# Performance work log

Measured on AMD Instinct MI355X. Metric: run time of the kernel, lower is better.

Reference implementation:

```python
import jax, jax.numpy as jnp
import numpy as np

EPS_FEAT = 1.0 + 1e-4   # feature_map offset: elu(x) + 1.0 + 0.0001
EPS_DEN = 1e-6


def setup_inputs() -> dict:
    key = jax.random.key(0)
    k1, k2, k3 = jax.random.split(key, 3)
    B, L, D = 4, 4096, 1024
    x = jax.random.normal(k1, (B, L, D), dtype=jnp.float32)
    # torch Linear-style init scale ~ 1/sqrt(fan_in)
    W_qkv = jax.random.normal(k2, (D, 3 * D), dtype=jnp.float32) / np.sqrt(D)
    b_qkv = jnp.zeros((3 * D,), dtype=jnp.float32)
    W_out = jax.random.normal(k3, (D, D), dtype=jnp.float32) / np.sqrt(D)
    b_out = jnp.zeros((D,), dtype=jnp.float32)
    return {"x": x, "W_qkv": W_qkv, "b_qkv": b_qkv, "W_out": W_out, "b_out": b_out}


def _linear_attention(x, W_qkv, b_qkv, W_out, b_out, num_heads=16):
    B, L, D = x.shape
    H = num_heads
    E = D // H

    qkv = x @ W_qkv + b_qkv                       # (B, L, 3D)
    q, k, v = jnp.split(qkv, 3, axis=-1)
    q = q.reshape(B, L, H, E)
    k = k.reshape(B, L, H, E)
    v = v.reshape(B, L, H, E)

    q = jax.nn.elu(q * (E ** -0.5)) + EPS_FEAT    # scale BEFORE feature map (as in source)
    k = jax.nn.elu(k) + EPS_FEAT

    # Causal linear attention via recurrence over L; math identical to
    # cumsum of k \otimes v outer products, but never materializes (B,L,H,E,E).
    qL = jnp.moveaxis(q, 1, 0)                    # (L, B, H, E)
    kL = jnp.moveaxis(k, 1, 0)
    vL = jnp.moveaxis(v, 1, 0)

    kv0 = jnp.zeros((B, H, E, E), dtype=x.dtype)
    ks0 = jnp.zeros((B, H, E), dtype=x.dtype)

    def step(carry, qkv_t):
        kv_s, k_s = carry
        q_t, k_t, v_t = qkv_t                     # each (B, H, E)
        kv_s = kv_s + jnp.einsum('bhe,bhf->bhef', k_t, v_t)
        k_s = k_s + k_t
        num = jnp.einsum('bhe,bhef->bhf', q_t, kv_s)           # (B, H, E)
        den = jnp.einsum('bhe,bhe->bh', q_t, k_s)[..., None] + EPS_DEN
        return (kv_s, k_s), num / den

    _, out = jax.lax.scan(step, (kv0, ks0), (qL, kL, vL))       # out: (L, B, H, E)
    out = jnp.moveaxis(out, 0, 1).reshape(B, L, D)
    # dropout is identity in eval mode
    return out @ W_out + b_out


def reference(x, W_qkv, b_qkv, W_out, b_out):
    return _linear_attention(x, W_qkv, b_qkv, W_out, b_out)
```

## Files before the change

### kernel.cpp

```cpp
#include <hip/hip_runtime.h>
#include <hip/hip_bf16.h>
#include <stdint.h>

#define B_ 4
#define L_ 4096
#define D_ 1024
#define H_ 16
#define E_ 64
#define M_ (B_*L_)
#define N1_ (3*D_)
#define CHK 128
#define NC (L_/CHK)
#define BH (B_*H_)

#define EPS_FEAT 1.0001f
#define EPS_DEN 1e-6f

typedef __attribute__((ext_vector_type(4))) float f32x4;
typedef __attribute__((ext_vector_type(8))) short bf16x8;

__device__ __forceinline__ unsigned short f2bf(float x) {
    union { float f; unsigned int u; } v; v.f = x;
    unsigned int r = v.u + 0x7FFFu + ((v.u >> 16) & 1u);
    return (unsigned short)(r >> 16);
}

__device__ __forceinline__ void gload_lds16(const unsigned short* g, unsigned short* l) {
    __builtin_amdgcn_global_load_lds(
        (const __attribute__((address_space(1))) unsigned int*)(const void*)g,
        (__attribute__((address_space(3))) unsigned int*)(void*)l,
        16, 0, 0);
}


__global__ __launch_bounds__(256) void cvt_x(const float* __restrict__ x,
                                             unsigned short* __restrict__ xb) {
    int i4 = blockIdx.x * 256 + threadIdx.x;
    float4 v = ((const float4*)x)[i4];
    unsigned int lo = (unsigned int)f2bf(v.x) | ((unsigned int)f2bf(v.y) << 16);
    unsigned int hi = (unsigned int)f2bf(v.z) | ((unsigned int)f2bf(v.w) << 16);
    ((uint2*)xb)[i4] = make_uint2(lo, hi);
}

__global__ __launch_bounds__(256) void transp_w(const float* __restrict__ W,
                                                unsigned short* __restrict__ WT,
                                                int K, int N) {
    __shared__ float tile[32][33];
    int kb = blockIdx.y * 32, nb = blockIdx.x * 32;
    int tx = threadIdx.x & 31, ty = threadIdx.x >> 5;
#pragma unroll
    for (int j = 0; j < 4; ++j)
        tile[ty + 8*j][tx] = W[(size_t)(kb + ty + 8*j) * N + nb + tx];
    __syncthreads();
#pragma unroll
    for (int j = 0; j < 4; ++j) {
        int nl = ty + 8*j;
        WT[(size_t)(nb + nl) * K + kb + tx] = f2bf(tile[tx][nl]);
    }
}


template<int MODE, int KDIM, int NDIM>
__global__ __launch_bounds__(512, 2) void gemm256(
    const unsigned short* __restrict__ A,
    const unsigned short* __restrict__ BT,
    const float* __restrict__ bias,
    float* __restrict__ outF,
    unsigned short* __restrict__ qf,
    unsigned short* __restrict__ kf,
    unsigned short* __restrict__ vf)
{
    __shared__ __align__(16) unsigned short smem[65536];

    const int t = threadIdx.x, lane = t & 63, w = t >> 6;
    const int wr = w >> 2, wc = w & 3;

    const int nwgx = NDIM / 256;
    const int nwg = nwgx * (M_ / 256);
    const int bid0 = blockIdx.y * nwgx + blockIdx.x;
    const int swz = (bid0 & 7) * (nwg >> 3) + (bid0 >> 3);
    const int m0 = (swz / nwgx) * 256, n0 = (swz % nwgx) * 256;
    const int lr = lane & 15, lg = lane >> 4;

    int srow[2], scol[2];
#pragma unroll
    for (int i = 0; i < 2; ++i) {
        int c = i * 512 + t;
        int row = c >> 2, s = c & 3;
        srow[i] = row;
        scol[i] = ((s ^ ((row >> 1) & 3)) << 3);
    }

    f32x4 acc[8][4] = {};

    auto stageHalf = [&](int T, int half) {
        unsigned short* base = smem + (T & 3) * 16384 + half * 8192;
        const unsigned short* src = half ? BT : A;
        const int boff = half ? n0 : m0;
        const int kt = T * 32;
#pragma unroll
        for (int i = 0; i < 2; ++i)
            gload_lds16(src + (size_t)(boff + srow[i]) * KDIM + kt + scol[i],
                        &base[(i*512 + t) * 8]);
    };

    auto tile = [&](int T, bool doStage) {
        const unsigned short* Ab = smem + (T & 3) * 16384;
        const unsigned short* Bb = Ab + 8192;
        bf16x8 af[4], bfr[4];
#pragma unroll
        for (int n = 0; n < 4; ++n) {
            int row = wc * 64 + n * 16 + lr;
            bfr[n] = *(const bf16x8*)&Bb[row * 32 + ((lg ^ ((row >> 1) & 3)) << 3)];
        }
#pragma unroll
        for (int m = 0; m < 4; ++m) {
            int row = wr * 128 + m * 16 + lr;
            af[m] = *(const bf16x8*)&Ab[row * 32 + ((lg ^ ((row >> 1) & 3)) << 3)];
        }
        if (doStage) stageHalf(T + 3, 0);
        __builtin_amdgcn_s_barrier();
        asm volatile("s_waitcnt lgkmcnt(0)" ::: "memory");
        __builtin_amdgcn_sched_barrier(0);
        __builtin_amdgcn_s_setprio(1);
#pragma unroll
        for (int m = 0; m < 4; ++m)
#pragma unroll
            for (int n = 0; n < 4; ++n)
                acc[m][n] = __builtin_amdgcn_mfma_f32_16x16x32_bf16(af[m], bfr[n], acc[m][n], 0, 0, 0);
        __builtin_amdgcn_s_setprio(0);
#pragma unroll
        for (int m = 0; m < 4; ++m) {
            int row = wr * 128 + (m + 4) * 16 + lr;
            af[m] = *(const bf16x8*)&Ab[row * 32 + ((lg ^ ((row >> 1) & 3)) << 3)];
        }
        if (doStage) stageHalf(T + 3, 1);
        __builtin_amdgcn_s_barrier();
        asm volatile("s_waitcnt lgkmcnt(0)" ::: "memory");
        __builtin_amdgcn_sched_barrier(0);
        __builtin_amdgcn_s_setprio(1);
#pragma unroll
        for (int m = 0; m < 4; ++m)
#pragma unroll
            for (int n = 0; n < 4; ++n)
                acc[m + 4][n] = __builtin_amdgcn_mfma_f32_16x16x32_bf16(af[m], bfr[n], acc[m + 4][n], 0, 0, 0);
        __builtin_amdgcn_s_setprio(0);
    };

    constexpr int NT = KDIM / 32;
    stageHalf(0,0); stageHalf(0,1);
    stageHalf(1,0); stageHalf(1,1);
    stageHalf(2,0); stageHalf(2,1);
    asm volatile("s_waitcnt vmcnt(8)" ::: "memory");
    __builtin_amdgcn_s_barrier();
    __builtin_amdgcn_sched_barrier(0);

    for (int T = 0; T <= NT - 4; ++T) {
        tile(T, true);
        asm volatile("s_waitcnt vmcnt(8)" ::: "memory");
        __builtin_amdgcn_s_barrier();
        __builtin_amdgcn_sched_barrier(0);
    }
    tile(NT - 3, false);
    asm volatile("s_waitcnt vmcnt(4)" ::: "memory");
    __builtin_amdgcn_s_barrier();
    __builtin_amdgcn_sched_barrier(0);
    tile(NT - 2, false);
    asm volatile("s_waitcnt vmcnt(0)" ::: "memory");
    __builtin_amdgcn_s_barrier();
    __builtin_amdgcn_sched_barrier(0);
    tile(NT - 1, false);
    __syncthreads();

    if (MODE == 0) {
        unsigned short* cbf = smem;
        const bool isQ = (n0 < D_), isK = (n0 >= D_ && n0 < 2*D_);
        const float scale = isQ ? 0.125f : 1.0f;
        unsigned short* buf = isQ ? qf : (isK ? kf : vf);
        const int b = m0 >> 12, l0 = m0 & 4095;
        const int h0 = (n0 & 1023) >> 6;
#pragma unroll
        for (int p = 0; p < 2; ++p) {
            if (wr == p) {
#pragma unroll
                for (int n = 0; n < 4; ++n) {
                    int cl = wc*64 + n*16 + lr;
                    float bv = bias[n0 + cl];
#pragma unroll
                    for (int m = 0; m < 8; ++m)
#pragma unroll
                        for (int q = 0; q < 4; ++q) {
                            int rl = m*16 + lg*4 + q;
                            float val = (acc[m][n][q] + bv) * scale;
                            float fv = (isQ || isK)
                                       ? ((val > 0.f ? val : __expf(val) - 1.f) + EPS_FEAT)
                                       : val;
                            cbf[rl * 264 + cl] = f2bf(fv);
                        }
                }
            }
            __syncthreads();
#pragma unroll
            for (int hh = 0; hh < 4; ++hh) {
                unsigned short* dst = buf + (((size_t)(b * H_ + h0 + hh)) * L_ + l0 + p*128) * E_;
#pragma unroll
                for (int i = 0; i < 2; ++i) {
                    int c = i*512 + t, row = c >> 3, ch = c & 7;
                    uint4 v = *(const uint4*)&cbf[row * 264 + hh*64 + ch*8];
                    *(uint4*)&dst[row * 64 + ch*8] = v;
                }
            }
            __syncthreads();
        }
    } else {
        float* cfl = (float*)smem;
#pragma unroll
        for (int p = 0; p < 4; ++p) {
            if (wr == (p >> 1)) {
                int mbase = (p & 1) * 4;
#pragma unroll
                for (int n = 0; n < 4; ++n) {
                    int cl = wc*64 + n*16 + lr;
                    float bv = bias[n0 + cl];
#pragma unroll
                    for (int mm = 0; mm < 4; ++mm)
#pragma unroll
                        for (int q = 0; q < 4; ++q) {
                            int rl = mm*16 + lg*4 + q;
                            cfl[rl * 260 + cl] = acc[mbase + mm][n][q] + bv;
                        }
                }
            }
            __syncthreads();
#pragma unroll
            for (int i = 0; i < 8; ++i) {
                int c = i*512 + t, row = c >> 6, ch = c & 63;
                float4 v = *(const float4*)&cfl[row * 260 + ch*4];
                *(float4*)&outF[(size_t)(m0 + p*64 + row) * NDIM + n0 + ch*4] = v;
            }
            __syncthreads();
        }
    }
}


__global__ __launch_bounds__(256) void chunk_kv(
    const unsigned short* __restrict__ kf, const unsigned short* __restrict__ vf,
    float* __restrict__ kvout, float* __restrict__ ksout)
{
    constexpr int LDK = 136;
    __shared__ unsigned short Kt[64 * LDK];
    __shared__ unsigned short Vt[80 * LDK];

    int t = threadIdx.x, lane = t & 63, w = t >> 6;
    int bid = blockIdx.x;
    const unsigned short* kp = kf + (size_t)bid * CHK * E_;
    const unsigned short* vp = vf + (size_t)bid * CHK * E_;

#pragma unroll
    for (int it = 0; it < 4; ++it) {
        int s = it * 256 + t;
        int rl = s >> 3, e0 = (s & 7) << 3;
        uint4 kv8 = *(const uint4*)(kp + s * 8);
        uint4 vv8 = *(const uint4*)(vp + s * 8);
        unsigned int kw[4] = {kv8.x, kv8.y, kv8.z, kv8.w};
        unsigned int vw[4] = {vv8.x, vv8.y, vv8.z, vv8.w};
#pragma unroll
        for (int jw = 0; jw < 4; ++jw) {
            Kt[(e0 + 2*jw    ) * LDK + rl] = (unsigned short)(kw[jw] & 0xFFFF);
            Kt[(e0 + 2*jw + 1) * LDK + rl] = (unsigned short)(kw[jw] >> 16);
            Vt[(e0 + 2*jw    ) * LDK + rl] = (unsigned short)(vw[jw] & 0xFFFF);
            Vt[(e0 + 2*jw + 1) * LDK + rl] = (unsigned short)(vw[jw] >> 16);
        }
    }
    if (t < 128) Vt[64 * LDK + t] = 0x3F80;
    for (int i = t; i < 15 * LDK; i += 256) Vt[65 * LDK + i] = 0;
    __syncthreads();

    int lr = lane & 15, lg = lane >> 4;
    f32x4 acc[5] = {};
#pragma unroll
    for (int ks = 0; ks < 4; ++ks) {
        bf16x8 a = *(const bf16x8*)&Kt[(w*16 + lr) * LDK + ks*32 + lg*8];
#pragma unroll
        for (int n = 0; n < 5; ++n) {
            bf16x8 b = *(const bf16x8*)&Vt[(n*16 + lr) * LDK + ks*32 + lg*8];
            acc[n] = __builtin_amdgcn_mfma_f32_16x16x32_bf16(a, b, acc[n], 0, 0, 0);
        }
    }
    float* kvo = kvout + (size_t)bid * E_ * E_;
#pragma unroll
    for (int n = 0; n < 4; ++n)
#pragma unroll
        for (int q = 0; q < 4; ++q) {
            int e = w*16 + lg*4 + q, f = n*16 + lr;
            kvo[e * 64 + f] = acc[n][q];
        }
    if (lr == 0) {
#pragma unroll
        for (int q = 0; q < 4; ++q) {
            int e = w*16 + lg*4 + q;
            ksout[(size_t)bid * 64 + e] = acc[4][q];
        }
    }
}


__global__ __launch_bounds__(256) void prefix_kv(
    const float* __restrict__ kv, const float* __restrict__ ks,
    unsigned short* __restrict__ kvb, unsigned short* __restrict__ ksb)
{
    int bh = blockIdx.y, part = blockIdx.x, t = threadIdx.x;
    float st[4];
#pragma unroll
    for (int j = 0; j < 4; ++j) st[j] = 0.f;
    for (int c = 0; c < NC; ++c) {
        const float* p = kv + ((size_t)bh * NC + c) * 4096 + part * 1024;
        unsigned short* q = kvb + ((size_t)bh * NC + c) * 4096 + part * 1024;
#pragma unroll
        for (int j = 0; j < 4; ++j) {
            float tmp = p[j * 256 + t];
            q[j * 256 + t] = f2bf(st[j]);
            st[j] += tmp;
        }
    }
    if (part == 0 && t < 64) {
        float s0 = 0.f;
        for (int c = 0; c < NC; ++c) {
            float tmp = ks[((size_t)bh * NC + c) * 64 + t];
            ksb[((size_t)bh * NC + c) * 64 + t] = f2bf(s0);
            s0 += tmp;
        }
    }
}


__global__ __launch_bounds__(256) void attn_out(
    const unsigned short* __restrict__ qf, const unsigned short* __restrict__ kf,
    const unsigned short* __restrict__ vf, const unsigned short* __restrict__ kvb,
    const unsigned short* __restrict__ ksb, unsigned short* __restrict__ attn)
{
    constexpr int LQ = 72;
    constexpr int LV = 136;
    constexpr int LKV = 72;
    __shared__ unsigned short Qs[128 * LQ];
    __shared__ unsigned short Ks[128 * LQ];
    __shared__ unsigned short Vt[80 * LV];
    __shared__ unsigned short KVt[80 * LKV];
    __shared__ unsigned short Ss[128 * LV];

    int t = threadIdx.x, lane = t & 63, w = t >> 6;
    int bid = blockIdx.x;
    int bh = bid >> 5, c = bid & 31;
    const unsigned short* qp = qf + (size_t)bid * CHK * E_;
    const unsigned short* kp = kf + (size_t)bid * CHK * E_;
    const unsigned short* vp = vf + (size_t)bid * CHK * E_;

#pragma unroll
    for (int it = 0; it < 4; ++it) {
        int s = it * 256 + t;
        int r = s >> 3, e0 = (s & 7) << 3;
        uint4 qv = *(const uint4*)(qp + s * 8);
        uint4 kv = *(const uint4*)(kp + s * 8);
        uint4 vv = *(const uint4*)(vp + s * 8);
        *(uint4*)&Qs[r * LQ + e0] = qv;
        *(uint4*)&Ks[r * LQ + e0] = kv;
        unsigned int vw[4] = {vv.x, vv.y, vv.z, vv.w};
#pragma unroll
        for (int jw = 0; jw < 4; ++jw) {
            Vt[(e0 + 2*jw    ) * LV + r] = (unsigned short)(vw[jw] & 0xFFFF);
            Vt[(e0 + 2*jw + 1) * LV + r] = (unsigned short)(vw[jw] >> 16);
        }
    }
    const unsigned short* kvp = kvb + (size_t)bid * 4096;
#pragma unroll
    for (int it = 0; it < 16; ++it) {
        int idx = it * 256 + t;
        int e = idx >> 6, f = idx & 63;
        KVt[f * LKV + e] = kvp[idx];
    }
    if (t < 64)  KVt[64 * LKV + t] = ksb[(size_t)bid * 64 + t];
    if (t < 128) Vt[64 * LV + t] = 0x3F80;
    for (int i = t; i < 15 * LV;  i += 256) Vt[65 * LV  + i] = 0;
    for (int i = t; i < 15 * LKV; i += 256) KVt[65 * LKV + i] = 0;
    __syncthreads();

    int lr = lane & 15, lg = lane >> 4;

#pragma unroll
    for (int m = 0; m < 2; ++m) {
        int rbase = w * 32 + m * 16;
        bf16x8 aq0 = *(const bf16x8*)&Qs[(rbase + lr) * LQ + lg*8];
        bf16x8 aq1 = *(const bf16x8*)&Qs[(rbase + lr) * LQ + 32 + lg*8];
        int jmax = 2 * w + m;
        for (int jb = 0; jb < 8; ++jb) {
            if (jb <= jmax) {
                f32x4 sacc = {};
                bf16x8 b0 = *(const bf16x8*)&Ks[(jb*16 + lr) * LQ + lg*8];
                bf16x8 b1 = *(const bf16x8*)&Ks[(jb*16 + lr) * LQ + 32 + lg*8];
                sacc = __builtin_amdgcn_mfma_f32_16x16x32_bf16(aq0, b0, sacc, 0, 0, 0);
                sacc = __builtin_amdgcn_mfma_f32_16x16x32_bf16(aq1, b1, sacc, 0, 0, 0);
#pragma unroll
                for (int q = 0; q < 4; ++q) {
                    int r = rbase + lg*4 + q;
                    int j = jb*16 + lr;
                    Ss[r * LV + j] = (j <= r) ? f2bf(sacc[q]) : (unsigned short)0;
                }
            } else {
#pragma unroll
                for (int q = 0; q < 4; ++q) {
                    int r = rbase + lg*4 + q;
                    Ss[r * LV + jb*16 + lr] = 0;
                }
            }
        }
    }

    f32x4 oacc[2][5] = {};
#pragma unroll
    for (int m = 0; m < 2; ++m) {
        int rbase = w * 32 + m * 16;
#pragma unroll
        for (int ks = 0; ks < 2; ++ks) {
            bf16x8 a = *(const bf16x8*)&Qs[(rbase + lr) * LQ + ks*32 + lg*8];
#pragma unroll
            for (int n = 0; n < 5; ++n) {
                bf16x8 b = *(const bf16x8*)&KVt[(n*16 + lr) * LKV + ks*32 + lg*8];
                oacc[m][n] = __builtin_amdgcn_mfma_f32_16x16x32_bf16(a, b, oacc[m][n], 0, 0, 0);
            }
        }
        for (int ks = 0; ks <= w; ++ks) {
            bf16x8 a = *(const bf16x8*)&Ss[(rbase + lr) * LV + ks*32 + lg*8];
#pragma unroll
            for (int n = 0; n < 5; ++n) {
                bf16x8 b = *(const bf16x8*)&Vt[(n*16 + lr) * LV + ks*32 + lg*8];
                oacc[m][n] = __builtin_amdgcn_mfma_f32_16x16x32_bf16(a, b, oacc[m][n], 0, 0, 0);
            }
        }
    }

    int b_idx = bh >> 4, h_idx = bh & 15;
#pragma unroll
    for (int m = 0; m < 2; ++m) {
        int rbase = w * 32 + m * 16;
        float den[4];
#pragma unroll
        for (int q = 0; q < 4; ++q)
            den[q] = __shfl(oacc[m][4][q], lane & 48, 64) + EPS_DEN;
#pragma unroll
        for (int n = 0; n < 4; ++n) {
#pragma unroll
            for (int q = 0; q < 4; ++q) {
                int r = rbase + lg*4 + q;
                int lpos = c * CHK + r;
                int col = n*16 + lr;
                size_t dst = ((size_t)b_idx * L_ + lpos) * D_ + h_idx * 64 + col;
                attn[dst] = f2bf(oacc[m][n][q] / den[q]);
            }
        }
    }
}


extern "C" void kernel_launch(void* const* d_in, const int* in_sizes, int n_in,
                              void* d_out, int out_size, void* d_ws, size_t ws_size,
                              hipStream_t stream)
{
    const float* x    = (const float*)d_in[0];
    const float* Wqkv = (const float*)d_in[1];
    const float* bqkv = (const float*)d_in[2];
    const float* Wout = (const float*)d_in[3];
    const float* bout = (const float*)d_in[4];
    float* out = (float*)d_out;

    char* ws = (char*)d_ws;
    size_t off = 0;
    auto alloc = [&](size_t bytes) { void* p = ws + off; off += (bytes + 255) & ~(size_t)255; return p; };
    unsigned short* xb  = (unsigned short*)alloc((size_t)M_ * D_ * 2);
    unsigned short* WqT = (unsigned short*)alloc((size_t)N1_ * D_ * 2);
    unsigned short* WoT = (unsigned short*)alloc((size_t)D_ * D_ * 2);
    unsigned short* qfb = (unsigned short*)alloc((size_t)M_ * D_ * 2);
    unsigned short* kfb = (unsigned short*)alloc((size_t)M_ * D_ * 2);
    unsigned short* vfb = (unsigned short*)alloc((size_t)M_ * D_ * 2);
    float* kvw = (float*)alloc((size_t)BH * NC * E_ * E_ * 4);
    float* ksw = (float*)alloc((size_t)BH * NC * E_ * 4);
    unsigned short* kvb = (unsigned short*)alloc((size_t)BH * NC * E_ * E_ * 2);
    unsigned short* ksb = (unsigned short*)alloc((size_t)BH * NC * E_ * 2);
    unsigned short* attn = xb;

    cvt_x<<<(M_ * D_ / 4) / 256, 256, 0, stream>>>(x, xb);
    transp_w<<<dim3(N1_ / 32, D_ / 32), 256, 0, stream>>>(Wqkv, WqT, D_, N1_);
    transp_w<<<dim3(D_ / 32, D_ / 32), 256, 0, stream>>>(Wout, WoT, D_, D_);

    gemm256<0, D_, N1_><<<dim3(N1_ / 256, M_ / 256), 512, 0, stream>>>(
        xb, WqT, bqkv, nullptr, qfb, kfb, vfb);

    chunk_kv<<<BH * NC, 256, 0, stream>>>(kfb, vfb, kvw, ksw);
    prefix_kv<<<dim3(4, BH), 256, 0, stream>>>(kvw, ksw, kvb, ksb);
    attn_out<<<BH * NC, 256, 0, stream>>>(qfb, kfb, vfb, kvb, ksb, attn);

    gemm256<1, D_, D_><<<dim3(D_ / 256, M_ / 256), 512, 0, stream>>>(
        attn, WoT, bout, out, nullptr, nullptr, nullptr);
}
```

Baseline: 282.4 us.

## Rework GEMM to K=64 double-buffered tiles and streamline chunked attention kernels

The GEMM main loop moves from a 4-stage ring of K=32 tiles to double-buffered K=64 tiles, with four MFMA phases per tile and a new XOR swizzle. chunk_kv writes the KV state transposed, so attn_out can read it directly from global memory instead of transposing it into shared memory. attn_out also keeps Q fragments in registers, builds the ones and ks columns as register fragments, and sets launch bounds for two blocks per CU. prefix_kv spreads work across four times as many blocks. Together these aim to cut LDS traffic and barrier overhead and to raise occupancy. The costs are fewer pipeline stages to hide global latency and more register pressure.

```diff
diff --git a/kernel.cpp b/kernel.cpp
--- a/kernel.cpp
+++ b/kernel.cpp
@@ -82,94 +82,114 @@
     const int m0 = (swz / nwgx) * 256, n0 = (swz % nwgx) * 256;
     const int lr = lane & 15, lg = lane >> 4;
 
-    int srow[2], scol[2];
-#pragma unroll
-    for (int i = 0; i < 2; ++i) {
-        int c = i * 512 + t;
-        int row = c >> 2, s = c & 3;
-        srow[i] = row;
-        scol[i] = ((s ^ ((row >> 1) & 3)) << 3);
-    }
-
+    auto stage = [&](int T, int ab, int h) {
+        unsigned short* base = smem + (T & 1) * 32768 + ab * 16384 + h * 8192;
+        const unsigned short* src = ab ? BT : A;
+        const int boff = (ab ? n0 : m0) + h * 128;
+        const int kt = T * 64;
+#pragma unroll
+        for (int i = 0; i < 2; ++i) {
+            int c = i * 512 + t;
+            int rowl = c >> 3, s = c & 7;
+            int col = ((s ^ (rowl & 7)) << 3);
+            gload_lds16(src + (size_t)(boff + rowl) * KDIM + kt + col, &base[c * 8]);
+        }
+    };
+
+    bf16x8 af[4][2], bq[4][2];
     f32x4 acc[8][4] = {};
 
-    auto stageHalf = [&](int T, int half) {
-        unsigned short* base = smem + (T & 3) * 16384 + half * 8192;
-        const unsigned short* src = half ? BT : A;
-        const int boff = half ? n0 : m0;
-        const int kt = T * 32;
-#pragma unroll
-        for (int i = 0; i < 2; ++i)
-            gload_lds16(src + (size_t)(boff + srow[i]) * KDIM + kt + scol[i],
-                        &base[(i*512 + t) * 8]);
+    auto rdA = [&](const unsigned short* Ab, int m, int ks) {
+        int row = wr * 128 + m * 16 + lr;
+        int slot = (ks * 4 + lg) ^ (row & 7);
+        return *(const bf16x8*)&Ab[row * 64 + slot * 8];
     };
-
-    auto tile = [&](int T, bool doStage) {
-        const unsigned short* Ab = smem + (T & 3) * 16384;
-        const unsigned short* Bb = Ab + 8192;
-        bf16x8 af[4], bfr[4];
-#pragma unroll
-        for (int n = 0; n < 4; ++n) {
-            int row = wc * 64 + n * 16 + lr;
-            bfr[n] = *(const bf16x8*)&Bb[row * 32 + ((lg ^ ((row >> 1) & 3)) << 3)];
-        }
-#pragma unroll
-        for (int m = 0; m < 4; ++m) {
-            int row = wr * 128 + m * 16 + lr;
-            af[m] = *(const bf16x8*)&Ab[row * 32 + ((lg ^ ((row >> 1) & 3)) << 3)];
-        }
-        if (doStage) stageHalf(T + 3, 0);
-        __builtin_amdgcn_s_barrier();
-        asm volatile("s_waitcnt lgkmcnt(0)" ::: "memory");
-        __builtin_amdgcn_sched_barrier(0);
-        __builtin_amdgcn_s_setprio(1);
+    auto rdB = [&](const unsigned short* Bb, int n, int ks) {
+        int row = wc * 64 + n * 16 + lr;
+        int slot = (ks * 4 + lg) ^ (row & 7);
+        return *(const bf16x8*)&Bb[row * 64 + slot * 8];
+    };
+
+#define PHASE_SYNC() \
+    __builtin_amdgcn_s_barrier(); \
+    asm volatile("s_waitcnt lgkmcnt(0)" ::: "memory"); \
+    __builtin_amdgcn_sched_barrier(0); \
+    __builtin_amdgcn_s_setprio(1);
+#define PHASE_END() \
+    __builtin_amdgcn_s_setprio(0); \
+    __builtin_amdgcn_s_barrier();
+
+    auto tile = [&](int T, bool s1, bool s2) {
+        const unsigned short* Ab = smem + (T & 1) * 32768;
+        const unsigned short* Bb = Ab + 16384;
+#pragma unroll
+        for (int m = 0; m < 4; ++m) { af[m][0] = rdA(Ab, m, 0); af[m][1] = rdA(Ab, m, 1); }
+#pragma unroll
+        for (int j = 0; j < 2; ++j) { bq[j][0] = rdB(Bb, j, 0); bq[j][1] = rdB(Bb, j, 1); }
+        if (s1) stage(T + 1, 0, 0);
+        PHASE_SYNC();
 #pragma unroll
         for (int m = 0; m < 4; ++m)
 #pragma unroll
-            for (int n = 0; n < 4; ++n)
-                acc[m][n] = __builtin_amdgcn_mfma_f32_16x16x32_bf16(af[m], bfr[n], acc[m][n], 0, 0, 0);
-        __builtin_amdgcn_s_setprio(0);
-#pragma unroll
-        for (int m = 0; m < 4; ++m) {
-            int row = wr * 128 + (m + 4) * 16 + lr;
-            af[m] = *(const bf16x8*)&Ab[row * 32 + ((lg ^ ((row >> 1) & 3)) << 3)];
-        }
-        if (doStage) stageHalf(T + 3, 1);
-        __builtin_amdgcn_s_barrier();
-        asm volatile("s_waitcnt lgkmcnt(0)" ::: "memory");
-        __builtin_amdgcn_sched_barrier(0);
-        __builtin_amdgcn_s_setprio(1);
+            for (int j = 0; j < 2; ++j) {
+                acc[m][j] = __builtin_amdgcn_mfma_f32_16x16x32_bf16(af[m][0], bq[j][0], acc[m][j], 0, 0, 0);
+                acc[m][j] = __builtin_amdgcn_mfma_f32_16x16x32_bf16(af[m][1], bq[j][1], acc[m][j], 0, 0, 0);
+            }
+        PHASE_END();
+#pragma unroll
+        for (int j = 0; j < 2; ++j) { bq[2+j][0] = rdB(Bb, 2+j, 0); bq[2+j][1] = rdB(Bb, 2+j, 1); }
+        if (s1) stage(T + 1, 0, 1);
+        PHASE_SYNC();
 #pragma unroll
         for (int m = 0; m < 4; ++m)
 #pragma unroll
-            for (int n = 0; n < 4; ++n)
-                acc[m + 4][n] = __builtin_amdgcn_mfma_f32_16x16x32_bf16(af[m], bfr[n], acc[m + 4][n], 0, 0, 0);
+            for (int j = 0; j < 2; ++j) {
+                acc[m][2+j] = __builtin_amdgcn_mfma_f32_16x16x32_bf16(af[m][0], bq[2+j][0], acc[m][2+j], 0, 0, 0);
+                acc[m][2+j] = __builtin_amdgcn_mfma_f32_16x16x32_bf16(af[m][1], bq[2+j][1], acc[m][2+j], 0, 0, 0);
+            }
+        PHASE_END();
+#pragma unroll
+        for (int m = 0; m < 4; ++m) { af[m][0] = rdA(Ab, 4+m, 0); af[m][1] = rdA(Ab, 4+m, 1); }
+        if (s2) stage(T + 2, 1, 0);
+        PHASE_SYNC();
+#pragma unroll
+        for (int m = 0; m < 4; ++m)
+#pragma unroll
+            for (int j = 0; j < 2; ++j) {
+                acc[4+m][j] = __builtin_amdgcn_mfma_f32_16x16x32_bf16(af[m][0], bq[j][0], acc[4+m][j], 0, 0, 0);
+                acc[4+m][j] = __builtin_amdgcn_mfma_f32_16x16x32_bf16(af[m][1], bq[j][1], acc[4+m][j], 0, 0, 0);
+            }
+        PHASE_END();
+        if (s2) stage(T + 2, 1, 1);
+        PHASE_SYNC();
+#pragma unroll
+        for (int m = 0; m < 4; ++m)
+#pragma unroll
+            for (int j = 0; j < 2; ++j) {
+                acc[4+m][2+j] = __builtin_amdgcn_mfma_f32_16x16x32_bf16(af[m][0], bq[2+j][0], acc[4+m][2+j], 0, 0, 0);
+                acc[4+m][2+j] = __builtin_amdgcn_mfma_f32_16x16x32_bf16(af[m][1], bq[2+j][1], acc[4+m][2+j], 0, 0, 0);
+            }
         __builtin_amdgcn_s_setprio(0);
     };
 
-    constexpr int NT = KDIM / 32;
-    stageHalf(0,0); stageHalf(0,1);
-    stageHalf(1,0); stageHalf(1,1);
-    stageHalf(2,0); stageHalf(2,1);
-    asm volatile("s_waitcnt vmcnt(8)" ::: "memory");
-    __builtin_amdgcn_s_barrier();
-    __builtin_amdgcn_sched_barrier(0);
-
-    for (int T = 0; T <= NT - 4; ++T) {
-        tile(T, true);
-        asm volatile("s_waitcnt vmcnt(8)" ::: "memory");
-        __builtin_amdgcn_s_barrier();
-        __builtin_amdgcn_sched_barrier(0);
-    }
-    tile(NT - 3, false);
+    constexpr int NT = KDIM / 64;
+    stage(0, 0, 0); stage(0, 0, 1); stage(0, 1, 0); stage(0, 1, 1);
+    stage(1, 1, 0); stage(1, 1, 1);
     asm volatile("s_waitcnt vmcnt(4)" ::: "memory");
     __builtin_amdgcn_s_barrier();
     __builtin_amdgcn_sched_barrier(0);
-    tile(NT - 2, false);
+
+    for (int T = 0; T < NT - 2; ++T) {
+        tile(T, true, T + 2 < NT);
+        asm volatile("s_waitcnt vmcnt(4)" ::: "memory");
+        __builtin_amdgcn_s_barrier();
+        __builtin_amdgcn_sched_barrier(0);
+    }
+    tile(NT - 2, true, false);
     asm volatile("s_waitcnt vmcnt(0)" ::: "memory");
     __builtin_amdgcn_s_barrier();
     __builtin_amdgcn_sched_barrier(0);
-    tile(NT - 1, false);
+    tile(NT - 1, false, false);
     __syncthreads();
 
     if (MODE == 0) {
@@ -241,6 +261,8 @@
             __syncthreads();
         }
     }
+#undef PHASE_SYNC
+#undef PHASE_END
 }
 
 
@@ -278,30 +300,40 @@
     __syncthreads();
 
     int lr = lane & 15, lg = lane >> 4;
-    f32x4 acc[5] = {};
+    f32x4 acc[4] = {};
+    f32x4 accE[4] = {};
 #pragma unroll
     for (int ks = 0; ks < 4; ++ks) {
-        bf16x8 a = *(const bf16x8*)&Kt[(w*16 + lr) * LDK + ks*32 + lg*8];
-#pragma unroll
-        for (int n = 0; n < 5; ++n) {
-            bf16x8 b = *(const bf16x8*)&Vt[(n*16 + lr) * LDK + ks*32 + lg*8];
+        bf16x8 a = *(const bf16x8*)&Vt[(w*16 + lr) * LDK + ks*32 + lg*8];
+#pragma unroll
+        for (int n = 0; n < 4; ++n) {
+            bf16x8 b = *(const bf16x8*)&Kt[(n*16 + lr) * LDK + ks*32 + lg*8];
             acc[n] = __builtin_amdgcn_mfma_f32_16x16x32_bf16(a, b, acc[n], 0, 0, 0);
         }
     }
+    if (w == 0) {
+#pragma unroll
+        for (int ks = 0; ks < 4; ++ks) {
+            bf16x8 a = *(const bf16x8*)&Vt[(64 + lr) * LDK + ks*32 + lg*8];
+#pragma unroll
+            for (int n = 0; n < 4; ++n) {
+                bf16x8 b = *(const bf16x8*)&Kt[(n*16 + lr) * LDK + ks*32 + lg*8];
+                accE[n] = __builtin_amdgcn_mfma_f32_16x16x32_bf16(a, b, accE[n], 0, 0, 0);
+            }
+        }
+    }
     float* kvo = kvout + (size_t)bid * E_ * E_;
 #pragma unroll
     for (int n = 0; n < 4; ++n)
 #pragma unroll
         for (int q = 0; q < 4; ++q) {
-            int e = w*16 + lg*4 + q, f = n*16 + lr;
-            kvo[e * 64 + f] = acc[n][q];
-        }
-    if (lr == 0) {
-#pragma unroll
-        for (int q = 0; q < 4; ++q) {
-            int e = w*16 + lg*4 + q;
-            ksout[(size_t)bid * 64 + e] = acc[4][q];
-        }
+            int f = w*16 + lg*4 + q, e = n*16 + lr;
+            kvo[f * 64 + e] = acc[n][q];
+        }
+    if (w == 0 && lg == 0) {
+#pragma unroll
+        for (int n = 0; n < 4; ++n)
+            ksout[(size_t)bid * 64 + n*16 + lr] = accE[n][0];
     }
 }
 
@@ -311,18 +343,12 @@
     unsigned short* __restrict__ kvb, unsigned short* __restrict__ ksb)
 {
     int bh = blockIdx.y, part = blockIdx.x, t = threadIdx.x;
-    float st[4];
-#pragma unroll
-    for (int j = 0; j < 4; ++j) st[j] = 0.f;
+    int idx = part * 256 + t;
+    float st = 0.f;
     for (int c = 0; c < NC; ++c) {
-        const float* p = kv + ((size_t)bh * NC + c) * 4096 + part * 1024;
-        unsigned short* q = kvb + ((size_t)bh * NC + c) * 4096 + part * 1024;
-#pragma unroll
-        for (int j = 0; j < 4; ++j) {
-            float tmp = p[j * 256 + t];
-            q[j * 256 + t] = f2bf(st[j]);
-            st[j] += tmp;
-        }
+        float tmp = kv[((size_t)bh * NC + c) * 4096 + idx];
+        kvb[((size_t)bh * NC + c) * 4096 + idx] = f2bf(st);
+        st += tmp;
     }
     if (part == 0 && t < 64) {
         float s0 = 0.f;
@@ -335,18 +361,15 @@
 }
 
 
-__global__ __launch_bounds__(256) void attn_out(
+__global__ __launch_bounds__(256, 2) void attn_out(
     const unsigned short* __restrict__ qf, const unsigned short* __restrict__ kf,
     const unsigned short* __restrict__ vf, const unsigned short* __restrict__ kvb,
     const unsigned short* __restrict__ ksb, unsigned short* __restrict__ attn)
 {
-    constexpr int LQ = 72;
+    constexpr int LK = 72;
     constexpr int LV = 136;
-    constexpr int LKV = 72;
-    __shared__ unsigned short Qs[128 * LQ];
-    __shared__ unsigned short Ks[128 * LQ];
-    __shared__ unsigned short Vt[80 * LV];
-    __shared__ unsigned short KVt[80 * LKV];
+    __shared__ unsigned short Ks[128 * LK];
+    __shared__ unsigned short Vt[64 * LV];
     __shared__ unsigned short Ss[128 * LV];
 
     int t = threadIdx.x, lane = t & 63, w = t >> 6;
@@ -355,16 +378,24 @@
     const unsigned short* qp = qf + (size_t)bid * CHK * E_;
     const unsigned short* kp = kf + (size_t)bid * CHK * E_;
     const unsigned short* vp = vf + (size_t)bid * CHK * E_;
+    const unsigned short* kvp = kvb + (size_t)bid * 4096;
+
+    int lr = lane & 15, lg = lane >> 4;
+
+    bf16x8 aq[2][2];
+#pragma unroll
+    for (int m = 0; m < 2; ++m)
+#pragma unroll
+        for (int ks = 0; ks < 2; ++ks)
+            aq[m][ks] = *(const bf16x8*)(qp + (w*32 + m*16 + lr) * 64 + ks*32 + lg*8);
 
 #pragma unroll
     for (int it = 0; it < 4; ++it) {
         int s = it * 256 + t;
         int r = s >> 3, e0 = (s & 7) << 3;
-        uint4 qv = *(const uint4*)(qp + s * 8);
         uint4 kv = *(const uint4*)(kp + s * 8);
         uint4 vv = *(const uint4*)(vp + s * 8);
-        *(uint4*)&Qs[r * LQ + e0] = qv;
-        *(uint4*)&Ks[r * LQ + e0] = kv;
+        *(uint4*)&Ks[r * LK + e0] = kv;
         unsigned int vw[4] = {vv.x, vv.y, vv.z, vv.w};
 #pragma unroll
         for (int jw = 0; jw < 4; ++jw) {
@@ -372,34 +403,27 @@
             Vt[(e0 + 2*jw + 1) * LV + r] = (unsigned short)(vw[jw] >> 16);
         }
     }
-    const unsigned short* kvp = kvb + (size_t)bid * 4096;
-#pragma unroll
-    for (int it = 0; it < 16; ++it) {
-        int idx = it * 256 + t;
-        int e = idx >> 6, f = idx & 63;
-        KVt[f * LKV + e] = kvp[idx];
-    }
-    if (t < 64)  KVt[64 * LKV + t] = ksb[(size_t)bid * 64 + t];
-    if (t < 128) Vt[64 * LV + t] = 0x3F80;
-    for (int i = t; i < 15 * LV;  i += 256) Vt[65 * LV  + i] = 0;
-    for (int i = t; i < 15 * LKV; i += 256) KVt[65 * LKV + i] = 0;
+    bf16x8 zfrag = {0,0,0,0,0,0,0,0};
+    bf16x8 bone = zfrag, bks[2] = {zfrag, zfrag};
+    if (lr == 0) {
+#pragma unroll
+        for (int j = 0; j < 8; ++j) bone[j] = (short)0x3F80;
+        bks[0] = *(const bf16x8*)&ksb[(size_t)bid * 64 + lg*8];
+        bks[1] = *(const bf16x8*)&ksb[(size_t)bid * 64 + 32 + lg*8];
+    }
     __syncthreads();
-
-    int lr = lane & 15, lg = lane >> 4;
 
 #pragma unroll
     for (int m = 0; m < 2; ++m) {
         int rbase = w * 32 + m * 16;
-        bf16x8 aq0 = *(const bf16x8*)&Qs[(rbase + lr) * LQ + lg*8];
-        bf16x8 aq1 = *(const bf16x8*)&Qs[(rbase + lr) * LQ + 32 + lg*8];
         int jmax = 2 * w + m;
         for (int jb = 0; jb < 8; ++jb) {
             if (jb <= jmax) {
                 f32x4 sacc = {};
-                bf16x8 b0 = *(const bf16x8*)&Ks[(jb*16 + lr) * LQ + lg*8];
-                bf16x8 b1 = *(const bf16x8*)&Ks[(jb*16 + lr) * LQ + 32 + lg*8];
-                sacc = __builtin_amdgcn_mfma_f32_16x16x32_bf16(aq0, b0, sacc, 0, 0, 0);
-                sacc = __builtin_amdgcn_mfma_f32_16x16x32_bf16(aq1, b1, sacc, 0, 0, 0);
+                bf16x8 b0 = *(const bf16x8*)&Ks[(jb*16 + lr) * LK + lg*8];
+                bf16x8 b1 = *(const bf16x8*)&Ks[(jb*16 + lr) * LK + 32 + lg*8];
+                sacc = __builtin_amdgcn_mfma_f32_16x16x32_bf16(aq[m][0], b0, sacc, 0, 0, 0);
+                sacc = __builtin_amdgcn_mfma_f32_16x16x32_bf16(aq[m][1], b1, sacc, 0, 0, 0);
 #pragma unroll
                 for (int q = 0; q < 4; ++q) {
                     int r = rbase + lg*4 + q;
@@ -422,20 +446,22 @@
         int rbase = w * 32 + m * 16;
 #pragma unroll
         for (int ks = 0; ks < 2; ++ks) {
-            bf16x8 a = *(const bf16x8*)&Qs[(rbase + lr) * LQ + ks*32 + lg*8];
-#pragma unroll
-            for (int n = 0; n < 5; ++n) {
-                bf16x8 b = *(const bf16x8*)&KVt[(n*16 + lr) * LKV + ks*32 + lg*8];
+            bf16x8 a = aq[m][ks];
+#pragma unroll
+            for (int n = 0; n < 4; ++n) {
+                bf16x8 b = *(const bf16x8*)&kvp[(n*16 + lr) * 64 + ks*32 + lg*8];
                 oacc[m][n] = __builtin_amdgcn_mfma_f32_16x16x32_bf16(a, b, oacc[m][n], 0, 0, 0);
             }
+            oacc[m][4] = __builtin_amdgcn_mfma_f32_16x16x32_bf16(a, bks[ks], oacc[m][4], 0, 0, 0);
         }
         for (int ks = 0; ks <= w; ++ks) {
             bf16x8 a = *(const bf16x8*)&Ss[(rbase + lr) * LV + ks*32 + lg*8];
 #pragma unroll
-            for (int n = 0; n < 5; ++n) {
+            for (int n = 0; n < 4; ++n) {
                 bf16x8 b = *(const bf16x8*)&Vt[(n*16 + lr) * LV + ks*32 + lg*8];
                 oacc[m][n] = __builtin_amdgcn_mfma_f32_16x16x32_bf16(a, b, oacc[m][n], 0, 0, 0);
             }
+            oacc[m][4] = __builtin_amdgcn_mfma_f32_16x16x32_bf16(a, bone, oacc[m][4], 0, 0, 0);
         }
     }
 
@@ -496,7 +522,7 @@
         xb, WqT, bqkv, nullptr, qfb, kfb, vfb);
 
     chunk_kv<<<BH * NC, 256, 0, stream>>>(kfb, vfb, kvw, ksw);
-    prefix_kv<<<dim3(4, BH), 256, 0, stream>>>(kvw, ksw, kvb, ksb);
+    prefix_kv<<<dim3(16, BH), 256, 0, stream>>>(kvw, ksw, kvb, ksb);
     attn_out<<<BH * NC, 256, 0, stream>>>(qfb, kfb, vfb, kvb, ksb, attn);
 
     gemm256<1, D_, D_><<<dim3(D_ / 256, M_ / 256), 512, 0, stream>>>(
```

Measured after the change: 249.2 us. 11.8% less time.
